# Optimization experiments

Measured on AMD Instinct MI355X. Metric: run time of the kernel, lower is better.

The kernel has to match this reference:

```python
import jax, jax.numpy as jnp
import numpy as np

B, S, H = 1, 2048, 1024
NQ, NKV, HD = 16, 8, 64
FF, E, TOPK = 2048, 4, 2
WINDOW = 512
CAP = 50.0
CLIP_L, CLIP_R = -0.03, 1.03
EPS = 1e-5
ROPE_BASE = 10000.0


def setup_inputs() -> dict:
    key = jax.random.key(0)
    ks = jax.random.split(key, 14)
    std = 0.02
    def nrm(k, shape):
        return jax.random.normal(k, shape, jnp.float32) * std
    return {
        'x': jax.random.normal(ks[0], (B, S, H), jnp.float32),
        'norm1_w': 1.0 + nrm(ks[1], (H,)),
        'wq': nrm(ks[2], (H, NQ * HD)),
        'wk': nrm(ks[3], (H, NKV * HD)),
        'wv': nrm(ks[4], (H, NKV * HD)),
        'wo': nrm(ks[5], (NQ * HD, H)),
        'qn_w': 1.0 + nrm(ks[6], (HD,)),
        'kn_w': 1.0 + nrm(ks[7], (HD,)),
        'norm2_w': 1.0 + nrm(ks[8], (H,)),
        'gate_w': nrm(ks[9], (H, E)),
        'w_gate': nrm(ks[10], (E, H, FF)),
        'w_up': nrm(ks[11], (E, H, FF)),
        'w_down': nrm(ks[12], (E, FF, H)),
    }


def _rms(x, w):
    return x * jax.lax.rsqrt(jnp.mean(x * x, axis=-1, keepdims=True) + EPS) * w


def _rope(t):
    # t: [B, S, N, D]
    D = t.shape[-1]
    half = D // 2
    inv = 1.0 / (ROPE_BASE ** (jnp.arange(half, dtype=jnp.float32) / half))
    ang = jnp.arange(t.shape[1], dtype=jnp.float32)[:, None] * inv  # [S, half]
    cos = jnp.cos(ang)[None, :, None, :]
    sin = jnp.sin(ang)[None, :, None, :]
    t1, t2 = t[..., :half], t[..., half:]
    return jnp.concatenate([t1 * cos - t2 * sin, t1 * sin + t2 * cos], axis=-1)


def reference(x, norm1_w, wq, wk, wv, wo, qn_w, kn_w, norm2_w, gate_w, w_gate, w_up, w_down):
    # --- self-attention block ---
    xn = _rms(x, norm1_w)
    q = (xn @ wq).reshape(B, S, NQ, HD)
    k = (xn @ wk).reshape(B, S, NKV, HD)
    v = (xn @ wv).reshape(B, S, NKV, HD)
    q = _rms(_rope(q), qn_w)  # RoPE then QK-norm over head_dim
    k = _rms(_rope(k), kn_w)
    rep = NQ // NKV
    k = jnp.repeat(k, rep, axis=2)  # GQA expand to NQ heads
    v = jnp.repeat(v, rep, axis=2)
    scale = 1.0 / np.sqrt(HD).astype(np.float32)
    scores = jnp.einsum('bqhd,bkhd->bhqk', q, k) * scale
    scores = CAP * jnp.tanh(scores / CAP)  # softmax capping (overrides temperature)
    i = jnp.arange(S)[:, None]
    j = jnp.arange(S)[None, :]
    allow = (j <= i) & (i - j < WINDOW)  # causal + sliding window
    scores = jnp.where(allow[None, None], scores, -jnp.inf)
    p = jax.nn.softmax(scores, axis=-1)
    p = jnp.clip((CLIP_R - CLIP_L) * p + CLIP_L, 0.0, 1.0)  # softmax clipping
    attn = jnp.einsum('bhqk,bkhd->bqhd', p, v).reshape(B, S, NQ * HD)
    h = x + attn @ wo
    # --- MoE gated-SiLU MLP block ---
    xn2 = _rms(h, norm2_w).reshape(B * S, H)
    probs = jax.nn.softmax(xn2 @ gate_w, axis=-1)
    topv, topi = jax.lax.top_k(probs, TOPK)
    topv = topv / jnp.sum(topv, axis=-1, keepdims=True)
    T = B * S
    wdense = jnp.zeros((T, E), jnp.float32).at[jnp.arange(T)[:, None], topi].add(topv)
    g = jnp.einsum('th,ehf->etf', xn2, w_gate)
    u = jnp.einsum('th,ehf->etf', xn2, w_up)
    y = jnp.einsum('etf,efh->eth', jax.nn.silu(g) * u, w_down)
    moe = jnp.einsum('eth,te->th', y, wdense)
    return h + moe.reshape(B, S, H)
```

## Files before the change

### kernel.cpp

```cpp
#include <hip/hip_runtime.h>
#include <hip/hip_bf16.h>
#include <math.h>

#define S_LEN   2048
#define H_DIM   1024
#define N_QH    16
#define N_KVH   8
#define HEADD   64
#define FF_DIM  2048
#define N_EXP   4
#define WIN     512
#define QB      16

typedef __attribute__((ext_vector_type(8))) short bf16x8;
typedef __attribute__((ext_vector_type(4))) float f32x4;

__device__ __forceinline__ short f2bf(float x) {
  unsigned u = __float_as_uint(x);
  u += 0x7fffu + ((u >> 16) & 1u);
  return (short)(u >> 16);
}
__device__ __forceinline__ float bf2f(short h) {
  return __uint_as_float((unsigned)(unsigned short)h << 16);
}
__device__ __forceinline__ int swz(int row, int col) {
  return row * 64 + (col ^ ((row & 7) << 3));
}

__global__ __launch_bounds__(256) void k_rope_tables(float* __restrict__ ct, float* __restrict__ st) {
  int i = blockIdx.x * 256 + threadIdx.x;
  int t = i >> 5, d = i & 31;
  double inv = 1.0 / pow(10000.0, (double)d / 32.0);
  double ang = (double)t * inv;
  ct[i] = (float)cos(ang);
  st[i] = (float)sin(ang);
}

template <int MODE>
__global__ __launch_bounds__(256) void k_rmsnorm(const float* __restrict__ x,
                                                 const float* __restrict__ w,
                                                 short* __restrict__ yh,
                                                 short* __restrict__ yl,
                                                 const float* __restrict__ gw,
                                                 float* __restrict__ wd) {
  int row = blockIdx.x;
  const float4 v = ((const float4*)(x + (long)row * H_DIM))[threadIdx.x];
  float ss = v.x * v.x + v.y * v.y + v.z * v.z + v.w * v.w;
  for (int off = 32; off; off >>= 1) ss += __shfl_xor(ss, off);
  __shared__ float red[4];
  if ((threadIdx.x & 63) == 0) red[threadIdx.x >> 6] = ss;
  __syncthreads();
  ss = red[0] + red[1] + red[2] + red[3];
  float r = (float)(1.0 / sqrt((double)ss * (1.0 / 1024.0) + 1e-5));
  const float4 wv = ((const float4*)w)[threadIdx.x];
  float4 o;
  o.x = v.x * r * wv.x; o.y = v.y * r * wv.y; o.z = v.z * r * wv.z; o.w = v.w * r * wv.w;
  if (MODE == 2) {
    short h0 = f2bf(o.x), h1 = f2bf(o.y), h2 = f2bf(o.z), h3 = f2bf(o.w);
    short l0 = f2bf(o.x - bf2f(h0)), l1 = f2bf(o.y - bf2f(h1));
    short l2 = f2bf(o.z - bf2f(h2)), l3 = f2bf(o.w - bf2f(h3));
    uint2 hv = make_uint2((unsigned short)h0 | ((unsigned)(unsigned short)h1 << 16),
                          (unsigned short)h2 | ((unsigned)(unsigned short)h3 << 16));
    uint2 lv = make_uint2((unsigned short)l0 | ((unsigned)(unsigned short)l1 << 16),
                          (unsigned short)l2 | ((unsigned)(unsigned short)l3 << 16));
    ((uint2*)(yh + (long)row * H_DIM))[threadIdx.x] = hv;
    ((uint2*)(yl + (long)row * H_DIM))[threadIdx.x] = lv;
  }
  if (MODE == 3) {
    unsigned lo = (unsigned short)f2bf(o.x) | ((unsigned)(unsigned short)f2bf(o.y) << 16);
    unsigned hi = (unsigned short)f2bf(o.z) | ((unsigned)(unsigned short)f2bf(o.w) << 16);
    ((uint2*)(yh + (long)row * H_DIM))[threadIdx.x] = make_uint2(lo, hi);
    int i0 = threadIdx.x * 4;
    float4 g0 = *(const float4*)&gw[(i0 + 0) * 4];
    float4 g1 = *(const float4*)&gw[(i0 + 1) * 4];
    float4 g2 = *(const float4*)&gw[(i0 + 2) * 4];
    float4 g3 = *(const float4*)&gw[(i0 + 3) * 4];
    float p0 = o.x * g0.x + o.y * g1.x + o.z * g2.x + o.w * g3.x;
    float p1 = o.x * g0.y + o.y * g1.y + o.z * g2.y + o.w * g3.y;
    float p2 = o.x * g0.z + o.y * g1.z + o.z * g2.z + o.w * g3.z;
    float p3 = o.x * g0.w + o.y * g1.w + o.z * g2.w + o.w * g3.w;
    for (int off = 32; off; off >>= 1) {
      p0 += __shfl_xor(p0, off); p1 += __shfl_xor(p1, off);
      p2 += __shfl_xor(p2, off); p3 += __shfl_xor(p3, off);
    }
    __shared__ float gred[4][4];
    int wid = threadIdx.x >> 6;
    if ((threadIdx.x & 63) == 0) { gred[wid][0] = p0; gred[wid][1] = p1; gred[wid][2] = p2; gred[wid][3] = p3; }
    __syncthreads();
    if (threadIdx.x == 0) {
      float l[4];
      for (int e = 0; e < 4; ++e) l[e] = gred[0][e] + gred[1][e] + gred[2][e] + gred[3][e];
      int i1 = 0;
      for (int e = 1; e < 4; ++e) if (l[e] > l[i1]) i1 = e;
      int i2 = -1;
      for (int e = 0; e < 4; ++e) { if (e == i1) continue; if (i2 < 0 || l[e] > l[i2]) i2 = e; }
      float e2 = expf(l[i2] - l[i1]);
      float w1 = 1.f / (1.f + e2);
      float ov[4] = {0.f, 0.f, 0.f, 0.f};
      ov[i1] = w1; ov[i2] = 1.f - w1;
      wd[row * 4 + 0] = ov[0]; wd[row * 4 + 1] = ov[1];
      wd[row * 4 + 2] = ov[2]; wd[row * 4 + 3] = ov[3];
    }
  }
}

__global__ __launch_bounds__(256) void k_tsplit(const float* __restrict__ in,
                                                short* __restrict__ oh,
                                                short* __restrict__ ol, int R, int C) {
  __shared__ float tile[32][33];
  int bx = blockIdx.x, by = blockIdx.y;
  int lx = threadIdx.x & 31, ly = threadIdx.x >> 5;
  int xc = bx * 32 + lx;
#pragma unroll
  for (int k = 0; k < 4; ++k) {
    int y = by * 32 + ly + k * 8;
    tile[ly + k * 8][lx] = in[(long)y * C + xc];
  }
  __syncthreads();
  int ox = by * 32 + lx;
#pragma unroll
  for (int k = 0; k < 4; ++k) {
    int oy = bx * 32 + ly + k * 8;
    float v = tile[lx][ly + k * 8];
    short hb = f2bf(v);
    short lb = f2bf(v - bf2f(hb));
    oh[(long)oy * R + ox] = hb;
    ol[(long)oy * R + ox] = lb;
  }
}

__global__ __launch_bounds__(256) void k_transpose_cast(const float* __restrict__ in,
                                                        short* __restrict__ out,
                                                        int R, int C) {
  __shared__ float tile[32][33];
  int bx = blockIdx.x, by = blockIdx.y;
  int lx = threadIdx.x & 31, ly = threadIdx.x >> 5;
  int x = bx * 32 + lx;
#pragma unroll
  for (int k = 0; k < 4; ++k) {
    int y = by * 32 + ly + k * 8;
    tile[ly + k * 8][lx] = in[(long)y * C + x];
  }
  __syncthreads();
  int ox = by * 32 + lx;
#pragma unroll
  for (int k = 0; k < 4; ++k) {
    int oy = bx * 32 + ly + k * 8;
    out[(long)oy * R + ox] = f2bf(tile[lx][ly + k * 8]);
  }
}

template <int ADD>
__global__ __launch_bounds__(256) void k_gemm_split(const short* __restrict__ Ah,
                                                    const short* __restrict__ Al,
                                                    const short* __restrict__ Bh,
                                                    const short* __restrict__ Bl,
                                                    const float* __restrict__ R,
                                                    float* __restrict__ C,
                                                    int K, int ldA, int ldB, int ldC) {
  __shared__ short AsH[128 * 64], AsL[128 * 64], BsH[128 * 64], BsL[128 * 64];
  const int r0 = blockIdx.x * 128, c0 = blockIdx.y * 128;
  const int tid = threadIdx.x;
  const int wid = tid >> 6, lane = tid & 63;
  const int wr = wid >> 1, wc = wid & 1;
  const int lr = lane & 15, lg = lane >> 4;
  f32x4 zero = {0.f, 0.f, 0.f, 0.f};
  f32x4 acc[4][4];
#pragma unroll
  for (int m = 0; m < 4; ++m)
#pragma unroll
    for (int n = 0; n < 4; ++n) acc[m][n] = zero;
  for (int k0 = 0; k0 < K; k0 += 64) {
#pragma unroll
    for (int it = 0; it < 4; ++it) {
      int flat = tid + it * 256;
      int row = flat >> 3, cb = (flat & 7) * 8;
      int d = swz(row, cb);
      *(uint4*)&AsH[d] = *(const uint4*)&Ah[(long)(r0 + row) * ldA + k0 + cb];
      *(uint4*)&AsL[d] = *(const uint4*)&Al[(long)(r0 + row) * ldA + k0 + cb];
      *(uint4*)&BsH[d] = *(const uint4*)&Bh[(long)(c0 + row) * ldB + k0 + cb];
      *(uint4*)&BsL[d] = *(const uint4*)&Bl[(long)(c0 + row) * ldB + k0 + cb];
    }
    __syncthreads();
#pragma unroll
    for (int kk = 0; kk < 64; kk += 32) {
      bf16x8 ah[4], al[4], bh[4], bl[4];
#pragma unroll
      for (int m = 0; m < 4; ++m) {
        int d = swz(wr * 64 + m * 16 + lr, kk + lg * 8);
        ah[m] = *(const bf16x8*)&AsH[d];
        al[m] = *(const bf16x8*)&AsL[d];
      }
#pragma unroll
      for (int n = 0; n < 4; ++n) {
        int d = swz(wc * 64 + n * 16 + lr, kk + lg * 8);
        bh[n] = *(const bf16x8*)&BsH[d];
        bl[n] = *(const bf16x8*)&BsL[d];
      }
#pragma unroll
      for (int m = 0; m < 4; ++m)
#pragma unroll
        for (int n = 0; n < 4; ++n) {
          acc[m][n] = __builtin_amdgcn_mfma_f32_16x16x32_bf16(ah[m], bh[n], acc[m][n], 0, 0, 0);
          acc[m][n] = __builtin_amdgcn_mfma_f32_16x16x32_bf16(ah[m], bl[n], acc[m][n], 0, 0, 0);
          acc[m][n] = __builtin_amdgcn_mfma_f32_16x16x32_bf16(al[m], bh[n], acc[m][n], 0, 0, 0);
        }
    }
    __syncthreads();
  }
#pragma unroll
  for (int m = 0; m < 4; ++m)
#pragma unroll
    for (int n = 0; n < 4; ++n) {
      int col = c0 + wc * 64 + n * 16 + lr;
#pragma unroll
      for (int r = 0; r < 4; ++r) {
        int row = r0 + wr * 64 + m * 16 + lg * 4 + r;
        float v = acc[m][n][r];
        if (ADD) v += R[(long)row * ldC + col];
        C[(long)row * ldC + col] = v;
      }
    }
}

__global__ __launch_bounds__(256) void k_rope_rms(float* __restrict__ qkv,
                                                  const float* __restrict__ qn_w,
                                                  const float* __restrict__ kn_w,
                                                  const float* __restrict__ ct,
                                                  const float* __restrict__ st) {
  int idx = blockIdx.x * 4 + (threadIdx.x >> 6);
  int lane = threadIdx.x & 63;
  int t = idx / 24, hh = idx - t * 24;
  long base; const float* w;
  if (hh < N_QH) { base = (long)t * 2048 + hh * HEADD;              w = qn_w; }
  else           { base = (long)t * 2048 + 1024 + (hh - N_QH) * HEADD; w = kn_w; }
  float x = qkv[base + lane];
  float partner = __shfl_xor(x, 32);
  int d = lane & 31;
  float cs = ct[t * 32 + d], sn = st[t * 32 + d];
  float r = x * cs + partner * ((lane < 32) ? -sn : sn);
  float ss = r * r;
  for (int off = 32; off; off >>= 1) ss += __shfl_xor(ss, off);
  float rr = (float)(1.0 / sqrt((double)ss * (1.0 / 64.0) + 1e-5));
  qkv[base + lane] = r * rr * w[lane];
}

__global__ __launch_bounds__(256) void k_attn(const float* __restrict__ qkv,
                                              short* __restrict__ attHi,
                                              short* __restrict__ attLo) {
  __shared__ float kv_s[64][68];
  __shared__ float sc[QB][584];
  __shared__ float row_a[QB];
  const int i0 = blockIdx.x * QB;
  const int hq = blockIdx.y;
  const int kvh = hq >> 1;
  const int tid = threadIdx.x;
  const int q = tid >> 4, cc = tid & 15;
  const int i = i0 + q;
  float4 qreg[16];
#pragma unroll
  for (int d4 = 0; d4 < 16; ++d4)
    qreg[d4] = *(const float4*)&qkv[(long)i * 2048 + hq * HEADD + d4 * 4];
  const int jstart = max(0, i0 - (WIN - 1));
  const int nch = (i0 + QB - jstart + 63) >> 6;
  for (int ch = 0; ch < nch; ++ch) {
    int jb = jstart + ch * 64;
#pragma unroll
    for (int it = 0; it < 4; ++it) {
      int flat4 = tid + it * 256;
      int r = flat4 >> 4, c4 = (flat4 & 15) * 4;
      int j = jb + r;
      float4 kvv = make_float4(0.f, 0.f, 0.f, 0.f);
      if (j < S_LEN) kvv = *(const float4*)&qkv[(long)j * 2048 + 1024 + kvh * HEADD + c4];
      *(float4*)&kv_s[r][c4] = kvv;
    }
    __syncthreads();
#pragma unroll
    for (int m = 0; m < 4; ++m) {
      int jl = cc + m * 16;
      int j = jb + jl;
      float s = 0.f;
#pragma unroll
      for (int d4 = 0; d4 < 16; ++d4) {
        float4 qv = qreg[d4];
        float4 kv = *(const float4*)&kv_s[jl][d4 * 4];
        s += qv.x * kv.x + qv.y * kv.y + qv.z * kv.z + qv.w * kv.w;
      }
      s *= 0.125f;
      s = 50.f * tanhf(s * 0.02f);
      bool allow = (j <= i) && (i - j < WIN);
      sc[q][ch * 64 + jl] = allow ? s : -1e30f;
    }
    __syncthreads();
  }
  {
    int wid = tid >> 6, lane = tid & 63;
    int ncols = nch * 64;
    for (int r = wid * 4; r < wid * 4 + 4; ++r) {
      float mx = -1e30f;
      for (int n = lane; n < ncols; n += 64) mx = fmaxf(mx, sc[r][n]);
      for (int off = 32; off; off >>= 1) mx = fmaxf(mx, __shfl_xor(mx, off));
      float sum = 0.f;
      for (int n = lane; n < ncols; n += 64) {
        float p = expf(sc[r][n] - mx);
        sc[r][n] = p; sum += p;
      }
      for (int off = 32; off; off >>= 1) sum += __shfl_xor(sum, off);
      if (lane == 0) row_a[r] = 1.06f / sum;
    }
  }
  __syncthreads();
  float outv[4] = {0.f, 0.f, 0.f, 0.f};
  for (int ch = 0; ch < nch; ++ch) {
    int jb = jstart + ch * 64;
#pragma unroll
    for (int it = 0; it < 4; ++it) {
      int flat4 = tid + it * 256;
      int r = flat4 >> 4, c4 = (flat4 & 15) * 4;
      int j = jb + r;
      float4 vv = make_float4(0.f, 0.f, 0.f, 0.f);
      if (j < S_LEN) vv = *(const float4*)&qkv[(long)j * 2048 + 1536 + kvh * HEADD + c4];
      *(float4*)&kv_s[r][c4] = vv;
    }
    __syncthreads();
    float a = row_a[q];
    for (int jl4 = 0; jl4 < 16; ++jl4) {
      float4 pp = *(const float4*)&sc[q][ch * 64 + jl4 * 4];
#pragma unroll
      for (int u = 0; u < 4; ++u) {
        float p = (&pp.x)[u];
        p = fminf(fmaxf(fmaf(a, p, -0.03f), 0.f), 1.f);
        float4 vv = *(const float4*)&kv_s[jl4 * 4 + u][cc * 4];
        outv[0] += p * vv.x; outv[1] += p * vv.y; outv[2] += p * vv.z; outv[3] += p * vv.w;
      }
    }
    __syncthreads();
  }
  long ob = (long)i * 1024 + hq * HEADD + cc * 4;
  short h0 = f2bf(outv[0]), h1 = f2bf(outv[1]), h2 = f2bf(outv[2]), h3 = f2bf(outv[3]);
  short l0 = f2bf(outv[0] - bf2f(h0)), l1 = f2bf(outv[1] - bf2f(h1));
  short l2 = f2bf(outv[2] - bf2f(h2)), l3 = f2bf(outv[3] - bf2f(h3));
  *(uint2*)&attHi[ob] = make_uint2((unsigned short)h0 | ((unsigned)(unsigned short)h1 << 16),
                                   (unsigned short)h2 | ((unsigned)(unsigned short)h3 << 16));
  *(uint2*)&attLo[ob] = make_uint2((unsigned short)l0 | ((unsigned)(unsigned short)l1 << 16),
                                   (unsigned short)l2 | ((unsigned)(unsigned short)l3 << 16));
}

template <int ATOMIC>
__global__ __launch_bounds__(256) void k_gemm_bf16(const short* __restrict__ A,
                                                   const short* __restrict__ Bt,
                                                   float* __restrict__ C,
                                                   int K, int ldA, int ldB, int ldC,
                                                   long sA, long sB, long sC) {
  __shared__ short As[128 * 64];
  __shared__ short Bs[128 * 64];
  const int e = blockIdx.z;
  A += (long)e * sA; Bt += (long)e * sB; C += (long)e * sC;
  const int r0 = blockIdx.x * 128, c0 = blockIdx.y * 128;
  const int tid = threadIdx.x;
  const int wid = tid >> 6, lane = tid & 63;
  const int wr = wid >> 1, wc = wid & 1;
  const int lr = lane & 15, lg = lane >> 4;
  f32x4 zero = {0.f, 0.f, 0.f, 0.f};
  f32x4 acc[4][4];
#pragma unroll
  for (int m = 0; m < 4; ++m)
#pragma unroll
    for (int n = 0; n < 4; ++n) acc[m][n] = zero;
  for (int k0 = 0; k0 < K; k0 += 64) {
#pragma unroll
    for (int it = 0; it < 4; ++it) {
      int flat = tid + it * 256;
      int row = flat >> 3, cb = (flat & 7) * 8;
      int d = swz(row, cb);
      *(uint4*)&As[d] = *(const uint4*)&A[(long)(r0 + row) * ldA + k0 + cb];
      *(uint4*)&Bs[d] = *(const uint4*)&Bt[(long)(c0 + row) * ldB + k0 + cb];
    }
    __syncthreads();
#pragma unroll
    for (int kk = 0; kk < 64; kk += 32) {
      bf16x8 af[4], bfr[4];
#pragma unroll
      for (int m = 0; m < 4; ++m) af[m] = *(const bf16x8*)&As[swz(wr * 64 + m * 16 + lr, kk + lg * 8)];
#pragma unroll
      for (int n = 0; n < 4; ++n) bfr[n] = *(const bf16x8*)&Bs[swz(wc * 64 + n * 16 + lr, kk + lg * 8)];
#pragma unroll
      for (int m = 0; m < 4; ++m)
#pragma unroll
        for (int n = 0; n < 4; ++n)
          acc[m][n] = __builtin_amdgcn_mfma_f32_16x16x32_bf16(af[m], bfr[n], acc[m][n], 0, 0, 0);
    }
    __syncthreads();
  }
#pragma unroll
  for (int m = 0; m < 4; ++m)
#pragma unroll
    for (int n = 0; n < 4; ++n) {
      int col = c0 + wc * 64 + n * 16 + lr;
#pragma unroll
      for (int r = 0; r < 4; ++r) {
        int row = r0 + wr * 64 + m * 16 + lg * 4 + r;
        float v = acc[m][n][r];
        if (ATOMIC) atomicAdd(&C[(long)row * ldC + col], v);
        else        C[(long)row * ldC + col] = v;
      }
    }
}

__global__ __launch_bounds__(256) void k_moe_act(const float* __restrict__ gu,
                                                 const float* __restrict__ wd,
                                                 short* __restrict__ aAll,
                                                 int e) {
  long i4 = (long)blockIdx.x * 256 + threadIdx.x;
  int t  = (int)(i4 >> 9);
  int f4 = (int)(i4 & 511);
  float wte = wd[t * 4 + e];
  float4 g = ((const float4*)gu)[(long)t * 1024 + f4];
  float4 u = ((const float4*)gu)[(long)t * 1024 + 512 + f4];
  float4 s;
  s.x = wte * u.x * g.x / (1.f + expf(-g.x));
  s.y = wte * u.y * g.y / (1.f + expf(-g.y));
  s.z = wte * u.z * g.z / (1.f + expf(-g.z));
  s.w = wte * u.w * g.w / (1.f + expf(-g.w));
  unsigned lo = (unsigned short)f2bf(s.x) | ((unsigned)(unsigned short)f2bf(s.y) << 16);
  unsigned hi = (unsigned short)f2bf(s.z) | ((unsigned)(unsigned short)f2bf(s.w) << 16);
  ((uint2*)(aAll + ((long)e << 22)))[i4] = make_uint2(lo, hi);
}

extern "C" void kernel_launch(void* const* d_in, const int* in_sizes, int n_in,
                              void* d_out, int out_size, void* d_ws, size_t ws_size,
                              hipStream_t stream) {
  const float* x       = (const float*)d_in[0];
  const float* norm1_w = (const float*)d_in[1];
  const float* wq      = (const float*)d_in[2];
  const float* wk      = (const float*)d_in[3];
  const float* wv      = (const float*)d_in[4];
  const float* wo      = (const float*)d_in[5];
  const float* qn_w    = (const float*)d_in[6];
  const float* kn_w    = (const float*)d_in[7];
  const float* norm2_w = (const float*)d_in[8];
  const float* gate_w  = (const float*)d_in[9];
  const float* w_gate  = (const float*)d_in[10];
  const float* w_up    = (const float*)d_in[11];
  const float* w_down  = (const float*)d_in[12];
  float* out = (float*)d_out;
  char* ws = (char*)d_ws;
  const unsigned long MB = 1ul << 20;

  float* ropeC = (float*)(ws + 0);
  float* ropeS = (float*)(ws + 256 * 1024);
  float* qkv   = (float*)(ws + 1 * MB);
  short* xnHi  = (short*)(ws + 17 * MB);
  short* xnLo  = (short*)(ws + 21 * MB);
  short* attHi = (short*)(ws + 25 * MB);
  short* attLo = (short*)(ws + 29 * MB);
  float* gu    = (float*)(ws + 1 * MB);
  short* qkvWh = (short*)(ws + 33 * MB);
  short* qkvWl = (short*)(ws + 37 * MB);
  short* woTh  = (short*)(ws + 41 * MB);
  short* woTl  = (short*)(ws + 43 * MB);
  float* h     = (float*)(ws + 45 * MB);
  short* guT   = (short*)(ws + 45 * MB);
  short* x2b   = (short*)(ws + 53 * MB);
  float* wd    = (float*)(ws + 57 * MB);
  short* dT    = (short*)(ws + 58 * MB);
  short* aAll  = (short*)(ws + 74 * MB);

  k_rope_tables<<<256, 256, 0, stream>>>(ropeC, ropeS);
  k_rmsnorm<2><<<S_LEN, 256, 0, stream>>>(x, norm1_w, xnHi, xnLo, nullptr, nullptr);
  k_tsplit<<<dim3(32, 32), 256, 0, stream>>>(wq, qkvWh, qkvWl, 1024, 1024);
  k_tsplit<<<dim3(16, 32), 256, 0, stream>>>(wk, qkvWh + 1024 * 1024, qkvWl + 1024 * 1024, 1024, 512);
  k_tsplit<<<dim3(16, 32), 256, 0, stream>>>(wv, qkvWh + 1536 * 1024, qkvWl + 1536 * 1024, 1024, 512);
  k_tsplit<<<dim3(32, 32), 256, 0, stream>>>(wo, woTh, woTl, 1024, 1024);
  k_gemm_split<0><<<dim3(16, 16), 256, 0, stream>>>(xnHi, xnLo, qkvWh, qkvWl, nullptr, qkv,
                                                    1024, 1024, 1024, 2048);
  k_rope_rms<<<(S_LEN * 24) / 4, 256, 0, stream>>>(qkv, qn_w, kn_w, ropeC, ropeS);
  k_attn<<<dim3(S_LEN / QB, N_QH), 256, 0, stream>>>(qkv, attHi, attLo);
  k_gemm_split<1><<<dim3(16, 8), 256, 0, stream>>>(attHi, attLo, woTh, woTl, x, h,
                                                   1024, 1024, 1024, 1024);
  k_rmsnorm<3><<<S_LEN, 256, 0, stream>>>(h, norm2_w, x2b, nullptr, gate_w, wd);
  hipMemcpyAsync(out, h, (size_t)S_LEN * H_DIM * sizeof(float), hipMemcpyDeviceToDevice, stream);
  for (int e = 0; e < N_EXP; ++e)
    k_transpose_cast<<<dim3(1024 / 32, 2048 / 32), 256, 0, stream>>>(
        w_down + (long)e * FF_DIM * H_DIM, dT + (long)e * H_DIM * FF_DIM, 2048, 1024);
  for (int e = 0; e < N_EXP; ++e) {
    k_transpose_cast<<<dim3(2048 / 32, 1024 / 32), 256, 0, stream>>>(
        w_gate + (long)e * H_DIM * FF_DIM, guT, 1024, 2048);
    k_transpose_cast<<<dim3(2048 / 32, 1024 / 32), 256, 0, stream>>>(
        w_up + (long)e * H_DIM * FF_DIM, guT + (long)FF_DIM * H_DIM, 1024, 2048);
    k_gemm_bf16<0><<<dim3(16, 32), 256, 0, stream>>>(x2b, guT, gu, 1024, 1024, 1024, 4096, 0, 0, 0);
    k_moe_act<<<4096, 256, 0, stream>>>(gu, wd, aAll, e);
  }
  k_gemm_bf16<1><<<dim3(16, 8, N_EXP), 256, 0, stream>>>(
      aAll, dT, out, 2048, 2048, 2048, 1024,
      (long)S_LEN * FF_DIM, (long)H_DIM * FF_DIM, 0);
}
```

Before: 716.6 us.

## Rewrite attention with bf16 split-precision MFMA for QK and PV

Replaces the scalar FP32 attention kernel with one that uses 16x16x32 bf16 MFMA instructions for both the QK^T scores and the P·V product. Q, K, V and the clipped probabilities are each split into hi/lo bf16 parts and combined with three MFMAs, which approximates FP32 accuracy. The intent is to move the attention dot products off vector ALUs onto matrix cores. In exchange it adds conversion work, a transposed V staging into shared memory with scalar loads, and extra packing passes over the score buffer.

After: 719.6 us. About the same (+0.4%).

```diff
diff --git a/kernel.cpp b/kernel.cpp
--- a/kernel.cpp
+++ b/kernel.cpp
@@ -245,105 +245,164 @@
   qkv[base + lane] = r * rr * w[lane];
 }
 
-__global__ __launch_bounds__(256) void k_attn(const float* __restrict__ qkv,
-                                              short* __restrict__ attHi,
-                                              short* __restrict__ attLo) {
-  __shared__ float kv_s[64][68];
-  __shared__ float sc[QB][584];
+__global__ __launch_bounds__(256) void k_attn_mfma(const float* __restrict__ qkv,
+                                                   short* __restrict__ attHi,
+                                                   short* __restrict__ attLo) {
+  __shared__ short Kh[64][72], Kl[64][72];
+  __shared__ float sc[QB][580];
   __shared__ float row_a[QB];
   const int i0 = blockIdx.x * QB;
   const int hq = blockIdx.y;
   const int kvh = hq >> 1;
   const int tid = threadIdx.x;
-  const int q = tid >> 4, cc = tid & 15;
-  const int i = i0 + q;
-  float4 qreg[16];
-#pragma unroll
-  for (int d4 = 0; d4 < 16; ++d4)
-    qreg[d4] = *(const float4*)&qkv[(long)i * 2048 + hq * HEADD + d4 * 4];
+  const int wv = tid >> 6, lane = tid & 63;
+  const int lr = lane & 15, lg = lane >> 4;
   const int jstart = max(0, i0 - (WIN - 1));
   const int nch = (i0 + QB - jstart + 63) >> 6;
+  const int ncols = nch * 64;
+  f32x4 zero = {0.f, 0.f, 0.f, 0.f};
+
+  bf16x8 qh[2], ql[2];
+  {
+    const float* qp = &qkv[(long)(i0 + lr) * 2048 + hq * HEADD];
+#pragma unroll
+    for (int kk = 0; kk < 2; ++kk) {
+      float4 f0 = *(const float4*)&qp[kk * 32 + lg * 8];
+      float4 f1 = *(const float4*)&qp[kk * 32 + lg * 8 + 4];
+      float ff[8] = {f0.x, f0.y, f0.z, f0.w, f1.x, f1.y, f1.z, f1.w};
+      bf16x8 h, l;
+#pragma unroll
+      for (int u = 0; u < 8; ++u) {
+        short hb = f2bf(ff[u]);
+        h[u] = hb; l[u] = f2bf(ff[u] - bf2f(hb));
+      }
+      qh[kk] = h; ql[kk] = l;
+    }
+  }
+
   for (int ch = 0; ch < nch; ++ch) {
     int jb = jstart + ch * 64;
-#pragma unroll
-    for (int it = 0; it < 4; ++it) {
-      int flat4 = tid + it * 256;
-      int r = flat4 >> 4, c4 = (flat4 & 15) * 4;
-      int j = jb + r;
-      float4 kvv = make_float4(0.f, 0.f, 0.f, 0.f);
-      if (j < S_LEN) kvv = *(const float4*)&qkv[(long)j * 2048 + 1024 + kvh * HEADD + c4];
-      *(float4*)&kv_s[r][c4] = kvv;
-    }
-    __syncthreads();
-#pragma unroll
-    for (int m = 0; m < 4; ++m) {
-      int jl = cc + m * 16;
-      int j = jb + jl;
-      float s = 0.f;
-#pragma unroll
-      for (int d4 = 0; d4 < 16; ++d4) {
-        float4 qv = qreg[d4];
-        float4 kv = *(const float4*)&kv_s[jl][d4 * 4];
-        s += qv.x * kv.x + qv.y * kv.y + qv.z * kv.z + qv.w * kv.w;
-      }
-      s *= 0.125f;
-      s = 50.f * tanhf(s * 0.02f);
+    {
+      int key = tid >> 2, dbase = (tid & 3) * 16;
+      int j = jb + key;
+      const float* kp = &qkv[(long)j * 2048 + 1024 + kvh * HEADD];
+#pragma unroll
+      for (int q4 = 0; q4 < 4; ++q4) {
+        int d = dbase + q4 * 4;
+        float4 f = make_float4(0.f, 0.f, 0.f, 0.f);
+        if (j < S_LEN) f = *(const float4*)&kp[d];
+        short h0 = f2bf(f.x), h1 = f2bf(f.y), h2 = f2bf(f.z), h3 = f2bf(f.w);
+        short l0 = f2bf(f.x - bf2f(h0)), l1 = f2bf(f.y - bf2f(h1));
+        short l2 = f2bf(f.z - bf2f(h2)), l3 = f2bf(f.w - bf2f(h3));
+        *(uint2*)&Kh[key][d] = make_uint2(
+            (unsigned short)h0 | ((unsigned)(unsigned short)h1 << 16),
+            (unsigned short)h2 | ((unsigned)(unsigned short)h3 << 16));
+        *(uint2*)&Kl[key][d] = make_uint2(
+            (unsigned short)l0 | ((unsigned)(unsigned short)l1 << 16),
+            (unsigned short)l2 | ((unsigned)(unsigned short)l3 << 16));
+      }
+    }
+    __syncthreads();
+    f32x4 s = zero;
+#pragma unroll
+    for (int kk = 0; kk < 2; ++kk) {
+      bf16x8 kh = *(const bf16x8*)&Kh[wv * 16 + lr][kk * 32 + lg * 8];
+      bf16x8 kl = *(const bf16x8*)&Kl[wv * 16 + lr][kk * 32 + lg * 8];
+      s = __builtin_amdgcn_mfma_f32_16x16x32_bf16(qh[kk], kh, s, 0, 0, 0);
+      s = __builtin_amdgcn_mfma_f32_16x16x32_bf16(qh[kk], kl, s, 0, 0, 0);
+      s = __builtin_amdgcn_mfma_f32_16x16x32_bf16(ql[kk], kh, s, 0, 0, 0);
+    }
+    int colbase = ch * 64 + wv * 16;
+#pragma unroll
+    for (int r = 0; r < 4; ++r) {
+      int q = 4 * lg + r;
+      int i = i0 + q;
+      int j = jb + wv * 16 + lr;
+      float v = s[r] * 0.125f;
+      v = 50.f * tanhf(v * 0.02f);
       bool allow = (j <= i) && (i - j < WIN);
-      sc[q][ch * 64 + jl] = allow ? s : -1e30f;
-    }
-    __syncthreads();
-  }
+      sc[q][colbase + lr] = allow ? v : -1e30f;
+    }
+    __syncthreads();
+  }
+
+  for (int r = wv * 4; r < wv * 4 + 4; ++r) {
+    float mx = -1e30f;
+    for (int n = lane; n < ncols; n += 64) mx = fmaxf(mx, sc[r][n]);
+    for (int off = 32; off; off >>= 1) mx = fmaxf(mx, __shfl_xor(mx, off));
+    float sum = 0.f;
+    for (int n = lane; n < ncols; n += 64) {
+      float p = expf(sc[r][n] - mx);
+      sc[r][n] = p; sum += p;
+    }
+    for (int off = 32; off; off >>= 1) sum += __shfl_xor(sum, off);
+    if (lane == 0) row_a[r] = 1.06f / sum;
+  }
+  __syncthreads();
+
   {
-    int wid = tid >> 6, lane = tid & 63;
-    int ncols = nch * 64;
-    for (int r = wid * 4; r < wid * 4 + 4; ++r) {
-      float mx = -1e30f;
-      for (int n = lane; n < ncols; n += 64) mx = fmaxf(mx, sc[r][n]);
-      for (int off = 32; off; off >>= 1) mx = fmaxf(mx, __shfl_xor(mx, off));
-      float sum = 0.f;
-      for (int n = lane; n < ncols; n += 64) {
-        float p = expf(sc[r][n] - mx);
-        sc[r][n] = p; sum += p;
-      }
-      for (int off = 32; off; off >>= 1) sum += __shfl_xor(sum, off);
-      if (lane == 0) row_a[r] = 1.06f / sum;
+    int q = tid >> 4;
+    float a = row_a[q];
+    for (int n = (tid & 15); n < ncols; n += 16) {
+      float e = sc[q][n];
+      float p = fminf(fmaxf(fmaf(a, e, -0.03f), 0.f), 1.f);
+      short ph = f2bf(p);
+      short pl = f2bf(p - bf2f(ph));
+      *(unsigned*)&sc[q][n] =
+          (unsigned)(unsigned short)ph | ((unsigned)(unsigned short)pl << 16);
     }
   }
   __syncthreads();
-  float outv[4] = {0.f, 0.f, 0.f, 0.f};
+
+  f32x4 oacc = zero;
   for (int ch = 0; ch < nch; ++ch) {
     int jb = jstart + ch * 64;
-#pragma unroll
-    for (int it = 0; it < 4; ++it) {
-      int flat4 = tid + it * 256;
-      int r = flat4 >> 4, c4 = (flat4 & 15) * 4;
-      int j = jb + r;
-      float4 vv = make_float4(0.f, 0.f, 0.f, 0.f);
-      if (j < S_LEN) vv = *(const float4*)&qkv[(long)j * 2048 + 1536 + kvh * HEADD + c4];
-      *(float4*)&kv_s[r][c4] = vv;
-    }
-    __syncthreads();
-    float a = row_a[q];
-    for (int jl4 = 0; jl4 < 16; ++jl4) {
-      float4 pp = *(const float4*)&sc[q][ch * 64 + jl4 * 4];
-#pragma unroll
-      for (int u = 0; u < 4; ++u) {
-        float p = (&pp.x)[u];
-        p = fminf(fmaxf(fmaf(a, p, -0.03f), 0.f), 1.f);
-        float4 vv = *(const float4*)&kv_s[jl4 * 4 + u][cc * 4];
-        outv[0] += p * vv.x; outv[1] += p * vv.y; outv[2] += p * vv.z; outv[3] += p * vv.w;
-      }
-    }
-    __syncthreads();
-  }
-  long ob = (long)i * 1024 + hq * HEADD + cc * 4;
-  short h0 = f2bf(outv[0]), h1 = f2bf(outv[1]), h2 = f2bf(outv[2]), h3 = f2bf(outv[3]);
-  short l0 = f2bf(outv[0] - bf2f(h0)), l1 = f2bf(outv[1] - bf2f(h1));
-  short l2 = f2bf(outv[2] - bf2f(h2)), l3 = f2bf(outv[3] - bf2f(h3));
-  *(uint2*)&attHi[ob] = make_uint2((unsigned short)h0 | ((unsigned)(unsigned short)h1 << 16),
-                                   (unsigned short)h2 | ((unsigned)(unsigned short)h3 << 16));
-  *(uint2*)&attLo[ob] = make_uint2((unsigned short)l0 | ((unsigned)(unsigned short)l1 << 16),
-                                   (unsigned short)l2 | ((unsigned)(unsigned short)l3 << 16));
+    {
+      int j = jb + (lane);
+      int dbase = wv * 16;
+      bool ok = (j < S_LEN);
+      const float* vp = &qkv[(long)j * 2048 + 1536 + kvh * HEADD];
+#pragma unroll
+      for (int dd = 0; dd < 16; ++dd) {
+        float f = ok ? vp[dbase + dd] : 0.f;
+        short hb = f2bf(f);
+        Kh[dbase + dd][lane] = hb;
+        Kl[dbase + dd][lane] = f2bf(f - bf2f(hb));
+      }
+    }
+    __syncthreads();
+#pragma unroll
+    for (int kk = 0; kk < 2; ++kk) {
+      const unsigned* pp = (const unsigned*)&sc[lr][ch * 64 + kk * 32 + lg * 8];
+      uint4 w0 = *(const uint4*)&pp[0];
+      uint4 w1 = *(const uint4*)&pp[4];
+      bf16x8 pa, pb;
+      pa[0] = (short)w0.x; pb[0] = (short)(w0.x >> 16);
+      pa[1] = (short)w0.y; pb[1] = (short)(w0.y >> 16);
+      pa[2] = (short)w0.z; pb[2] = (short)(w0.z >> 16);
+      pa[3] = (short)w0.w; pb[3] = (short)(w0.w >> 16);
+      pa[4] = (short)w1.x; pb[4] = (short)(w1.x >> 16);
+      pa[5] = (short)w1.y; pb[5] = (short)(w1.y >> 16);
+      pa[6] = (short)w1.z; pb[6] = (short)(w1.z >> 16);
+      pa[7] = (short)w1.w; pb[7] = (short)(w1.w >> 16);
+      bf16x8 vh = *(const bf16x8*)&Kh[wv * 16 + lr][kk * 32 + lg * 8];
+      bf16x8 vl = *(const bf16x8*)&Kl[wv * 16 + lr][kk * 32 + lg * 8];
+      oacc = __builtin_amdgcn_mfma_f32_16x16x32_bf16(pa, vh, oacc, 0, 0, 0);
+      oacc = __builtin_amdgcn_mfma_f32_16x16x32_bf16(pa, vl, oacc, 0, 0, 0);
+      oacc = __builtin_amdgcn_mfma_f32_16x16x32_bf16(pb, vh, oacc, 0, 0, 0);
+    }
+    __syncthreads();
+  }
+#pragma unroll
+  for (int r = 0; r < 4; ++r) {
+    int q = 4 * lg + r;
+    int d = wv * 16 + lr;
+    long ob = (long)(i0 + q) * 1024 + hq * HEADD + d;
+    float v = oacc[r];
+    short hb = f2bf(v);
+    attHi[ob] = hb;
+    attLo[ob] = f2bf(v - bf2f(hb));
+  }
 }
 
 template <int ATOMIC>
@@ -475,7 +534,7 @@
   k_gemm_split<0><<<dim3(16, 16), 256, 0, stream>>>(xnHi, xnLo, qkvWh, qkvWl, nullptr, qkv,
                                                     1024, 1024, 1024, 2048);
   k_rope_rms<<<(S_LEN * 24) / 4, 256, 0, stream>>>(qkv, qn_w, kn_w, ropeC, ropeS);
-  k_attn<<<dim3(S_LEN / QB, N_QH), 256, 0, stream>>>(qkv, attHi, attLo);
+  k_attn_mfma<<<dim3(S_LEN / QB, N_QH), 256, 0, stream>>>(qkv, attHi, attLo);
   k_gemm_split<1><<<dim3(16, 8), 256, 0, stream>>>(attHi, attLo, woTh, woTl, x, h,
                                                    1024, 1024, 1024, 1024);
   k_rmsnorm<3><<<S_LEN, 256, 0, stream>>>(h, norm2_w, x2b, nullptr, gate_w, wd);
```
